# Performance work log

Hardware: AMD Instinct MI355X
Metric: run time of the kernel (lower is better)

## Reference

```python
import jax, jax.numpy as jnp
import numpy as np

B, T, HID = 4, 16, 4096
H, D = 32, 128
S_PAST = 4096


def setup_inputs() -> dict:
    key = jax.random.key(0)
    ks = jax.random.split(key, 7)
    w_scale = 0.02  # keep logits/activations numerically tame
    return {
        "hidden": jax.random.normal(ks[0], (B, T, HID), dtype=jnp.float32),
        "cache_k": jax.random.normal(ks[1], (B, H, S_PAST, D), dtype=jnp.float32),
        "cache_v": jax.random.normal(ks[2], (B, H, S_PAST, D), dtype=jnp.float32),
        "wq": jax.random.normal(ks[3], (HID, HID), dtype=jnp.float32) * w_scale,
        "wk": jax.random.normal(ks[4], (HID, HID), dtype=jnp.float32) * w_scale,
        "wv": jax.random.normal(ks[5], (HID, HID), dtype=jnp.float32) * w_scale,
        "wo": jax.random.normal(ks[6], (HID, HID), dtype=jnp.float32) * w_scale,
    }


def reference(hidden, cache_k, cache_v, wq, wk, wv, wo):
    b, t, _ = hidden.shape
    # QKV projections (torch Linear: x @ W.T), reshape to [B,H,T,D]
    q = (hidden @ wq.T).reshape(b, t, H, D).transpose(0, 2, 1, 3)
    k_new = (hidden @ wk.T).reshape(b, t, H, D).transpose(0, 2, 1, 3)
    v_new = (hidden @ wv.T).reshape(b, t, H, D).transpose(0, 2, 1, 3)
    # DynamicCache append-by-concat
    k_full = jnp.concatenate([cache_k, k_new], axis=2)  # [B,H,S+T,D]
    v_full = jnp.concatenate([cache_v, v_new], axis=2)
    # SDPA, non-causal (torch default), scale = 1/sqrt(D)
    scale = 1.0 / jnp.sqrt(jnp.asarray(D, dtype=q.dtype))
    scores = jnp.einsum("bhtd,bhsd->bhts", q, k_full) * scale
    attn = jax.nn.softmax(scores, axis=-1)
    ctx = jnp.einsum("bhts,bhsd->bhtd", attn, v_full)  # [B,H,T,D]
    out = ctx.transpose(0, 2, 1, 3).reshape(b, t, H * D) @ wo.T
    return out, k_full, v_full
```

## Files before the change

### kernel.cpp

```cpp
#include <hip/hip_runtime.h>
#include <hip/hip_bf16.h>
#include <math.h>

#define HIDN  4096
#define NH    32
#define HD    128
#define NB    4
#define NT    16
#define MM    64
#define SPAST 4096
#define STOT  4112
#define NCHUNK 8
#define SCHUNK 514

#define WS_Q    0
#define WS_CTX  262144
#define WS_PART 524288
#define PART_STRIDE 2080

typedef float f32x4 __attribute__((ext_vector_type(4)));
typedef short bf16x8 __attribute__((ext_vector_type(8)));

__device__ __forceinline__ bf16x8 load_bf16x8(const float* p) {
    const float4* p4 = (const float4*)p;
    float4 a = p4[0], b = p4[1];
    float f[8] = {a.x, a.y, a.z, a.w, b.x, b.y, b.z, b.w};
    union { unsigned short u[8]; bf16x8 v; } r;
#pragma unroll
    for (int i = 0; i < 8; ++i) {
        unsigned int x = __float_as_uint(f[i]);
        r.u[i] = (unsigned short)((x + 0x7FFFu + ((x >> 16) & 1u)) >> 16);
    }
    return r.v;
}

__global__ __launch_bounds__(256) void gemm64_kernel(
    const float* __restrict__ A,
    const float* __restrict__ w0, const float* __restrict__ w1, const float* __restrict__ w2,
    float* __restrict__ c0, float* __restrict__ c1, float* __restrict__ c2)
{
    const int wave = threadIdx.x >> 6;
    const int lane = threadIdx.x & 63;
    const int l16  = lane & 15;
    const int quad = lane >> 4;
    const int y = blockIdx.y;
    const float* W = (y == 0) ? w0 : (y == 1) ? w1 : w2;
    float*       C = (y == 0) ? c0 : (y == 1) ? c1 : c2;

    const int n = blockIdx.x * 64 + wave * 16 + l16;
    const float* wrow  = W + (size_t)n * HIDN + quad * 8;
    const float* arow0 = A + (size_t)l16 * HIDN + quad * 8;

    f32x4 acc[4] = {};
    for (int k0 = 0; k0 < HIDN; k0 += 32) {
        bf16x8 bfrag = load_bf16x8(wrow + k0);
#pragma unroll
        for (int mi = 0; mi < 4; ++mi) {
            bf16x8 afrag = load_bf16x8(arow0 + (size_t)mi * 16 * HIDN + k0);
            acc[mi] = __builtin_amdgcn_mfma_f32_16x16x32_bf16(afrag, bfrag, acc[mi], 0, 0, 0);
        }
    }
#pragma unroll
    for (int mi = 0; mi < 4; ++mi) {
#pragma unroll
        for (int r = 0; r < 4; ++r) {
            int m = mi * 16 + quad * 4 + r;
            if (y == 0) {
                C[(size_t)m * HIDN + n] = acc[mi][r];
            } else {
                int b = m >> 4, t = m & 15, h = n >> 7, d = n & 127;
                C[((size_t)(b * NH + h) * STOT + SPAST + t) * HD + d] = acc[mi][r];
            }
        }
    }
}

__global__ __launch_bounds__(256) void concat_copy_kernel(
    const float4* __restrict__ ck, float4* __restrict__ kf,
    const float4* __restrict__ cv, float4* __restrict__ vf)
{
    const float4* src = blockIdx.y ? cv : ck;
    float4*       dst = blockIdx.y ? vf : kf;
    const long long total = 16777216LL;
    for (long long i = (long long)blockIdx.x * blockDim.x + threadIdx.x; i < total;
         i += (long long)gridDim.x * blockDim.x) {
        long long bh = i >> 17;
        long long r  = i & 131071LL;
        dst[bh * 131584LL + r] = src[i];
    }
}

__global__ __launch_bounds__(256) void attn_partial_kernel(
    const float* __restrict__ qp,
    const float* __restrict__ kf,
    const float* __restrict__ vf,
    float* __restrict__ part)
{
    __shared__ float qs[16][128];
    __shared__ float sc[16][257];
    __shared__ float red[16][16];
    __shared__ float m_run[16], l_run[16], alpha_s[16];

    const int tid = threadIdx.x;
    const int bh  = blockIdx.x;
    const int c   = blockIdx.y;
    const int b = bh >> 5, h = bh & 31;
    const int s_beg = c * SCHUNK, s_end = s_beg + SCHUNK;

    const float scale = 0.08838834764831845f;
    for (int i = tid; i < 16 * 128; i += 256) {
        int t = i >> 7, d = i & 127;
        qs[t][d] = qp[(size_t)(b * 16 + t) * HIDN + h * 128 + d] * scale;
    }
    if (tid < 16) { m_run[tid] = -INFINITY; l_run[tid] = 0.f; }
    __syncthreads();

    const int tg = tid >> 4;
    const int ig = tid & 15;
    float o_loc[8];
#pragma unroll
    for (int i = 0; i < 8; ++i) o_loc[i] = 0.f;

    for (int s0 = s_beg; s0 < s_end; s0 += 256) {
        const int tile_n = min(256, s_end - s0);
        if (tid < tile_n) {
            const float* krow = kf + ((size_t)bh * STOT + (s0 + tid)) * HD;
            float scr[16];
#pragma unroll
            for (int t = 0; t < 16; ++t) scr[t] = 0.f;
            for (int dc = 0; dc < 128; dc += 32) {
                float4 kb[8];
#pragma unroll
                for (int u = 0; u < 8; ++u) kb[u] = ((const float4*)(krow + dc))[u];
#pragma unroll
                for (int t = 0; t < 16; ++t) {
                    float s4 = 0.f;
#pragma unroll
                    for (int u = 0; u < 8; ++u) {
                        float4 qv = ((const float4*)&qs[t][dc])[u];
                        s4 += qv.x * kb[u].x + qv.y * kb[u].y + qv.z * kb[u].z + qv.w * kb[u].w;
                    }
                    scr[t] += s4;
                }
            }
#pragma unroll
            for (int t = 0; t < 16; ++t) sc[t][tid] = scr[t];
        }
        __syncthreads();
        {
            float pm = -INFINITY;
            for (int j = ig; j < tile_n; j += 16) pm = fmaxf(pm, sc[tg][j]);
            red[tg][ig] = pm;
        }
        __syncthreads();
        if (tid < 16) {
            float tmax = -INFINITY;
#pragma unroll
            for (int i = 0; i < 16; ++i) tmax = fmaxf(tmax, red[tid][i]);
            float mo = m_run[tid];
            float mn = fmaxf(mo, tmax);
            alpha_s[tid] = __expf(mo - mn);
            m_run[tid] = mn;
        }
        __syncthreads();
        {
            float ps = 0.f;
            const float mn = m_run[tg];
            for (int j = ig; j < tile_n; j += 16) {
                float p = __expf(sc[tg][j] - mn);
                sc[tg][j] = p;
                ps += p;
            }
            red[tg][ig] = ps;
        }
        __syncthreads();
        if (tid < 16) {
            float ts = 0.f;
#pragma unroll
            for (int i = 0; i < 16; ++i) ts += red[tid][i];
            l_run[tid] = l_run[tid] * alpha_s[tid] + ts;
        }
        __syncthreads();
        {
            const float al = alpha_s[tg];
#pragma unroll
            for (int i = 0; i < 8; ++i) o_loc[i] *= al;
            const float* vbase = vf + ((size_t)bh * STOT + s0) * HD + ig * 8;
            for (int j = 0; j < tile_n; ++j) {
                float p = sc[tg][j];
                const float4* vr = (const float4*)(vbase + (size_t)j * HD);
                float4 v0 = vr[0], v1 = vr[1];
                o_loc[0] += p * v0.x; o_loc[1] += p * v0.y;
                o_loc[2] += p * v0.z; o_loc[3] += p * v0.w;
                o_loc[4] += p * v1.x; o_loc[5] += p * v1.y;
                o_loc[6] += p * v1.z; o_loc[7] += p * v1.w;
            }
        }
        __syncthreads();
    }
    float* pp = part + ((size_t)bh * NCHUNK + c) * PART_STRIDE;
#pragma unroll
    for (int i = 0; i < 8; ++i) pp[tg * 128 + ig * 8 + i] = o_loc[i];
    if (tid < 16) { pp[2048 + tid] = m_run[tid]; pp[2064 + tid] = l_run[tid]; }
}

__global__ __launch_bounds__(256) void combine_kernel(
    const float* __restrict__ part, float* __restrict__ ctx)
{
    const int bh = blockIdx.x;
    const int tid = threadIdx.x;
    const int t = tid >> 4, i = tid & 15;
    const int b = bh >> 5, h = bh & 31;
    const float* pb = part + (size_t)bh * NCHUNK * PART_STRIDE;

    float M = -INFINITY;
#pragma unroll
    for (int cI = 0; cI < NCHUNK; ++cI) M = fmaxf(M, pb[cI * PART_STRIDE + 2048 + t]);
    float L = 0.f;
    float w[NCHUNK];
#pragma unroll
    for (int cI = 0; cI < NCHUNK; ++cI) {
        float e = __expf(pb[cI * PART_STRIDE + 2048 + t] - M);
        w[cI] = e;
        L += e * pb[cI * PART_STRIDE + 2064 + t];
    }
    const float invL = 1.f / L;
    float o[8];
#pragma unroll
    for (int k = 0; k < 8; ++k) o[k] = 0.f;
#pragma unroll
    for (int cI = 0; cI < NCHUNK; ++cI) {
        const float* po = pb + cI * PART_STRIDE + t * 128 + i * 8;
        const float wc = w[cI];
#pragma unroll
        for (int k = 0; k < 8; ++k) o[k] += wc * po[k];
    }
    float* dst = ctx + (size_t)(b * 16 + t) * HIDN + h * 128 + i * 8;
#pragma unroll
    for (int k = 0; k < 8; ++k) dst[k] = o[k] * invL;
}

extern "C" void kernel_launch(void* const* d_in, const int* in_sizes, int n_in,
                              void* d_out, int out_size, void* d_ws, size_t ws_size,
                              hipStream_t stream) {
    const float* hidden  = (const float*)d_in[0];
    const float* cache_k = (const float*)d_in[1];
    const float* cache_v = (const float*)d_in[2];
    const float* wq = (const float*)d_in[3];
    const float* wk = (const float*)d_in[4];
    const float* wv = (const float*)d_in[5];
    const float* wo = (const float*)d_in[6];

    float* out   = (float*)d_out;
    float* kfull = out + 262144;
    float* vfull = kfull + 67371008LL;

    float* ws   = (float*)d_ws;
    float* qp   = ws + WS_Q;
    float* ctx  = ws + WS_CTX;
    float* part = ws + WS_PART;

    gemm64_kernel<<<dim3(64, 3), 256, 0, stream>>>(hidden, wq, wk, wv, qp, kfull, vfull);
    concat_copy_kernel<<<dim3(4096, 2), 256, 0, stream>>>(
        (const float4*)cache_k, (float4*)kfull, (const float4*)cache_v, (float4*)vfull);
    attn_partial_kernel<<<dim3(128, NCHUNK), 256, 0, stream>>>(qp, kfull, vfull, part);
    combine_kernel<<<dim3(128), 256, 0, stream>>>(part, ctx);
    gemm64_kernel<<<dim3(64, 1), 256, 0, stream>>>(ctx, wo, wo, wo, out, nullptr, nullptr);
}
```

Baseline: 1.506 ms.

## Fuse KV cache concat copy into attention and retile projection GEMM

```diff
diff --git a/kernel.cpp b/kernel.cpp
--- a/kernel.cpp
+++ b/kernel.cpp
@@ -7,11 +7,9 @@
 #define HD    128
 #define NB    4
 #define NT    16
-#define MM    64
 #define SPAST 4096
 #define STOT  4112
 #define NCHUNK 8
-#define SCHUNK 514
 
 #define WS_Q    0
 #define WS_CTX  262144
@@ -24,13 +22,11 @@
 __device__ __forceinline__ bf16x8 load_bf16x8(const float* p) {
     const float4* p4 = (const float4*)p;
     float4 a = p4[0], b = p4[1];
-    float f[8] = {a.x, a.y, a.z, a.w, b.x, b.y, b.z, b.w};
-    union { unsigned short u[8]; bf16x8 v; } r;
-#pragma unroll
-    for (int i = 0; i < 8; ++i) {
-        unsigned int x = __float_as_uint(f[i]);
-        r.u[i] = (unsigned short)((x + 0x7FFFu + ((x >> 16) & 1u)) >> 16);
-    }
+    union { __hip_bfloat162 h[4]; bf16x8 v; } r;
+    r.h[0] = __float22bfloat162_rn(make_float2(a.x, a.y));
+    r.h[1] = __float22bfloat162_rn(make_float2(a.z, a.w));
+    r.h[2] = __float22bfloat162_rn(make_float2(b.x, b.y));
+    r.h[3] = __float22bfloat162_rn(make_float2(b.z, b.w));
     return r.v;
 }
 
@@ -39,7 +35,7 @@
     const float* __restrict__ w0, const float* __restrict__ w1, const float* __restrict__ w2,
     float* __restrict__ c0, float* __restrict__ c1, float* __restrict__ c2)
 {
-    const int wave = threadIdx.x >> 6;
+    const int mi   = threadIdx.x >> 6;
     const int lane = threadIdx.x & 63;
     const int l16  = lane & 15;
     const int quad = lane >> 4;
@@ -47,53 +43,35 @@
     const float* W = (y == 0) ? w0 : (y == 1) ? w1 : w2;
     float*       C = (y == 0) ? c0 : (y == 1) ? c1 : c2;
 
-    const int n = blockIdx.x * 64 + wave * 16 + l16;
-    const float* wrow  = W + (size_t)n * HIDN + quad * 8;
-    const float* arow0 = A + (size_t)l16 * HIDN + quad * 8;
-
-    f32x4 acc[4] = {};
+    const int n = blockIdx.x * 16 + l16;
+    const float* wrow = W + (size_t)n * HIDN + quad * 8;
+    const float* arow = A + (size_t)(mi * 16 + l16) * HIDN + quad * 8;
+
+    f32x4 acc = {};
+#pragma unroll 4
     for (int k0 = 0; k0 < HIDN; k0 += 32) {
         bf16x8 bfrag = load_bf16x8(wrow + k0);
-#pragma unroll
-        for (int mi = 0; mi < 4; ++mi) {
-            bf16x8 afrag = load_bf16x8(arow0 + (size_t)mi * 16 * HIDN + k0);
-            acc[mi] = __builtin_amdgcn_mfma_f32_16x16x32_bf16(afrag, bfrag, acc[mi], 0, 0, 0);
-        }
-    }
-#pragma unroll
-    for (int mi = 0; mi < 4; ++mi) {
-#pragma unroll
-        for (int r = 0; r < 4; ++r) {
-            int m = mi * 16 + quad * 4 + r;
-            if (y == 0) {
-                C[(size_t)m * HIDN + n] = acc[mi][r];
-            } else {
-                int b = m >> 4, t = m & 15, h = n >> 7, d = n & 127;
-                C[((size_t)(b * NH + h) * STOT + SPAST + t) * HD + d] = acc[mi][r];
-            }
-        }
-    }
-}
-
-__global__ __launch_bounds__(256) void concat_copy_kernel(
-    const float4* __restrict__ ck, float4* __restrict__ kf,
-    const float4* __restrict__ cv, float4* __restrict__ vf)
-{
-    const float4* src = blockIdx.y ? cv : ck;
-    float4*       dst = blockIdx.y ? vf : kf;
-    const long long total = 16777216LL;
-    for (long long i = (long long)blockIdx.x * blockDim.x + threadIdx.x; i < total;
-         i += (long long)gridDim.x * blockDim.x) {
-        long long bh = i >> 17;
-        long long r  = i & 131071LL;
-        dst[bh * 131584LL + r] = src[i];
+        bf16x8 afrag = load_bf16x8(arow + k0);
+        acc = __builtin_amdgcn_mfma_f32_16x16x32_bf16(afrag, bfrag, acc, 0, 0, 0);
+    }
+#pragma unroll
+    for (int r = 0; r < 4; ++r) {
+        int m = mi * 16 + quad * 4 + r;
+        if (y == 0) {
+            C[(size_t)m * HIDN + n] = acc[r];
+        } else {
+            int b = m >> 4, t = m & 15, h = n >> 7, d = n & 127;
+            C[((size_t)(b * NH + h) * STOT + SPAST + t) * HD + d] = acc[r];
+        }
     }
 }
 
 __global__ __launch_bounds__(256) void attn_partial_kernel(
     const float* __restrict__ qp,
-    const float* __restrict__ kf,
-    const float* __restrict__ vf,
+    const float* __restrict__ ck,
+    const float* __restrict__ cv,
+    float* __restrict__ kf,
+    float* __restrict__ vf,
     float* __restrict__ part)
 {
     __shared__ float qs[16][128];
@@ -105,7 +83,8 @@
     const int bh  = blockIdx.x;
     const int c   = blockIdx.y;
     const int b = bh >> 5, h = bh & 31;
-    const int s_beg = c * SCHUNK, s_end = s_beg + SCHUNK;
+    const int s_beg = c * 512;
+    const int s_end = (c == NCHUNK - 1) ? STOT : (s_beg + 512);
 
     const float scale = 0.08838834764831845f;
     for (int i = tid; i < 16 * 128; i += 256) {
@@ -123,8 +102,12 @@
 
     for (int s0 = s_beg; s0 < s_end; s0 += 256) {
         const int tile_n = min(256, s_end - s0);
+        const bool is_new = (s0 >= SPAST);
         if (tid < tile_n) {
-            const float* krow = kf + ((size_t)bh * STOT + (s0 + tid)) * HD;
+            const int s = s0 + tid;
+            const float* krow = is_new ? (kf + ((size_t)bh * STOT  + s) * HD)
+                                       : (ck + ((size_t)bh * SPAST + s) * HD);
+            float* kdst = kf + ((size_t)bh * STOT + s) * HD;
             float scr[16];
 #pragma unroll
             for (int t = 0; t < 16; ++t) scr[t] = 0.f;
@@ -132,6 +115,10 @@
                 float4 kb[8];
 #pragma unroll
                 for (int u = 0; u < 8; ++u) kb[u] = ((const float4*)(krow + dc))[u];
+                if (!is_new) {
+#pragma unroll
+                    for (int u = 0; u < 8; ++u) ((float4*)(kdst + dc))[u] = kb[u];
+                }
 #pragma unroll
                 for (int t = 0; t < 16; ++t) {
                     float s4 = 0.f;
@@ -185,11 +172,17 @@
             const float al = alpha_s[tg];
 #pragma unroll
             for (int i = 0; i < 8; ++i) o_loc[i] *= al;
-            const float* vbase = vf + ((size_t)bh * STOT + s0) * HD + ig * 8;
+            const float* vsrc = is_new ? (vf + ((size_t)bh * STOT  + s0) * HD)
+                                       : (cv + ((size_t)bh * SPAST + s0) * HD);
+            float* vdst = vf + ((size_t)bh * STOT + s0) * HD;
             for (int j = 0; j < tile_n; ++j) {
                 float p = sc[tg][j];
-                const float4* vr = (const float4*)(vbase + (size_t)j * HD);
+                const float4* vr = (const float4*)(vsrc + (size_t)j * HD + ig * 8);
                 float4 v0 = vr[0], v1 = vr[1];
+                if (!is_new && ((j & 15) == tg)) {
+                    float4* vw = (float4*)(vdst + (size_t)j * HD + ig * 8);
+                    vw[0] = v0; vw[1] = v1;
+                }
                 o_loc[0] += p * v0.x; o_loc[1] += p * v0.y;
                 o_loc[2] += p * v0.z; o_loc[3] += p * v0.w;
                 o_loc[4] += p * v1.x; o_loc[5] += p * v1.y;
@@ -260,10 +253,9 @@
     float* ctx  = ws + WS_CTX;
     float* part = ws + WS_PART;
 
-    gemm64_kernel<<<dim3(64, 3), 256, 0, stream>>>(hidden, wq, wk, wv, qp, kfull, vfull);
-    concat_copy_kernel<<<dim3(4096, 2), 256, 0, stream>>>(
-        (const float4*)cache_k, (float4*)kfull, (const float4*)cache_v, (float4*)vfull);
-    attn_partial_kernel<<<dim3(128, NCHUNK), 256, 0, stream>>>(qp, kfull, vfull, part);
+    gemm64_kernel<<<dim3(256, 3), 256, 0, stream>>>(hidden, wq, wk, wv, qp, kfull, vfull);
+    attn_partial_kernel<<<dim3(128, NCHUNK), 256, 0, stream>>>(
+        qp, cache_k, cache_v, kfull, vfull, part);
     combine_kernel<<<dim3(128), 256, 0, stream>>>(part, ctx);
-    gemm64_kernel<<<dim3(64, 1), 256, 0, stream>>>(ctx, wo, wo, wo, out, nullptr, nullptr);
-}
+    gemm64_kernel<<<dim3(256, 1), 256, 0, stream>>>(ctx, wo, wo, wo, out, nullptr, nullptr);
+}
```

New measurement: 1.419 ms. 1.06x faster.
